# Optimization experiments

Measured on AMD Instinct MI355X. Metric: run time of the kernel, lower is better.

The kernel has to match this reference:

```python
import jax, jax.numpy as jnp
import numpy as np

B = 1024        # number of graphs
MAXLEN = 64     # max nodes per graph (pad_sequence length)
E = 256         # hidden_size
H = 8           # num_heads
HD = E // H     # head dim
NEG = -1e9


def setup_inputs() -> dict:
    key = jax.random.key(0)
    k0, k1, k2 = jax.random.split(key, 3)
    lens = np.tile(np.array([32, 48, 64, 40], dtype=np.int64), B // 4)  # sum = 47104
    batch_indices = jnp.asarray(np.repeat(np.arange(B, dtype=np.int64), lens))
    N = int(lens.sum())
    node_features = jax.random.normal(k0, (N, E), dtype=jnp.float32)
    in_proj_w = jax.random.normal(k1, (3 * E, E), dtype=jnp.float32) * (1.0 / np.sqrt(E))
    in_proj_b = jnp.zeros((3 * E,), dtype=jnp.float32)
    out_proj_w = jax.random.normal(k2, (E, E), dtype=jnp.float32) * (1.0 / np.sqrt(E))
    out_proj_b = jnp.zeros((E,), dtype=jnp.float32)
    return {"node_features": node_features, "batch_indices": batch_indices,
            "in_proj_w": in_proj_w, "in_proj_b": in_proj_b,
            "out_proj_w": out_proj_w, "out_proj_b": out_proj_b}


def _pad_ragged(node_features, batch_indices):
    # counts per graph, start offset of each graph, position of each node in its graph
    N = node_features.shape[0]
    counts = jax.ops.segment_sum(jnp.ones((N,), jnp.int32), batch_indices, num_segments=B)
    starts = jnp.cumsum(counts) - counts
    pos = jnp.arange(N) - starts[batch_indices]
    padded = jnp.zeros((B, MAXLEN, E), node_features.dtype).at[batch_indices, pos].set(node_features)
    key_pad = jnp.arange(MAXLEN)[None, :] >= counts[:, None]  # [B, L] True = padding
    return padded, key_pad


def reference(node_features, batch_indices, in_proj_w, in_proj_b, out_proj_w, out_proj_b):
    padded, key_pad = _pad_ragged(node_features, batch_indices)   # [B,L,E], [B,L]
    qkv = padded @ in_proj_w.T + in_proj_b                        # [B,L,3E]
    q, k, v = jnp.split(qkv, 3, axis=-1)
    q = q.reshape(B, MAXLEN, H, HD)
    k = k.reshape(B, MAXLEN, H, HD)
    v = v.reshape(B, MAXLEN, H, HD)
    scores = jnp.einsum('blhd,bmhd->bhlm', q, k) / jnp.sqrt(jnp.float32(HD))
    scores = jnp.where(key_pad[:, None, None, :], NEG, scores)    # mask padded keys
    attn = jax.nn.softmax(scores, axis=-1)                        # [B,H,L,L]
    ctx = jnp.einsum('bhlm,bmhd->blhd', attn, v).reshape(B, MAXLEN, E)
    out = ctx @ out_proj_w.T + out_proj_b                         # [B,L,E]
    out = jnp.transpose(out, (1, 0, 2))                           # [L,B,E] seq-first like torch
    weights = attn.mean(axis=1)                                   # [B,L,L] head-averaged
    return out, weights
```

## Files before the change

### kernel.cpp

```cpp
#include <hip/hip_runtime.h>

typedef unsigned short u16;
typedef short bf16x8 __attribute__((ext_vector_type(8)));
typedef float f32x4 __attribute__((ext_vector_type(4)));

#define MFMA16(a, b, c) __builtin_amdgcn_mfma_f32_16x16x32_bf16((a), (b), (c), 0, 0, 0)

static __device__ __forceinline__ u16 f2bf(float f) {
    union { float f; unsigned int u; } v; v.f = f;
    unsigned int u = v.u;
    u += 0x7fffu + ((u >> 16) & 1u);
    return (u16)(u >> 16);
}

__global__ void prep_kernel(const int* __restrict__ bidx, int N,
                            const float* __restrict__ w_in, const float* __restrict__ w_out,
                            int* __restrict__ starts, int* __restrict__ counts,
                            u16* __restrict__ w_in_bf, u16* __restrict__ w_out_bf) {
    int tid = blockIdx.x * blockDim.x + threadIdx.x;
    if (tid < 1024) {
        int lo = 0, hi = N;
        while (lo < hi) { int mid = (lo + hi) >> 1; if (bidx[mid] < tid) lo = mid + 1; else hi = mid; }
        int s0 = lo;
        lo = 0; hi = N;
        int v1 = tid + 1;
        while (lo < hi) { int mid = (lo + hi) >> 1; if (bidx[mid] < v1) lo = mid + 1; else hi = mid; }
        starts[tid] = s0;
        counts[tid] = lo - s0;
    }
    {
        float4 v = ((const float4*)w_in)[tid];
        ushort4 o; o.x = f2bf(v.x); o.y = f2bf(v.y); o.z = f2bf(v.z); o.w = f2bf(v.w);
        ((ushort4*)w_in_bf)[tid] = o;
    }
    if (tid < 16384) {
        float4 v = ((const float4*)w_out)[tid];
        ushort4 o; o.x = f2bf(v.x); o.y = f2bf(v.y); o.z = f2bf(v.z); o.w = f2bf(v.w);
        ((ushort4*)w_out_bf)[tid] = o;
    }
}

__global__ __launch_bounds__(256, 2) void gat_kernel(
    const float* __restrict__ X, const float* __restrict__ bias_in,
    const float* __restrict__ bias_out,
    const int* __restrict__ starts, const int* __restrict__ counts,
    const u16* __restrict__ w_in_bf, const u16* __restrict__ w_out_bf,
    float* __restrict__ out, float* __restrict__ wout) {

    __shared__ u16 qg[64][72];
    __shared__ u16 kg[64][72];
    __shared__ u16 vt[64][72];
    __shared__ u16 p_s[4][16][72];
    __shared__ u16 cs[64][264];

    const int b = blockIdx.x;
    const int tid = threadIdx.x;
    const int w = tid >> 6;
    const int lane = tid & 63;
    const int n = lane & 15;
    const int quad = lane >> 4;
    const int s = starts[b];
    const int c = counts[b];
    const int m0 = w * 16;

    bf16x8 afr[4][8];
    #pragma unroll
    for (int st = 0; st < 4; ++st) {
        int row = st * 16 + n;
        bool ok = row < c;
        const float* src = X + (long)(s + row) * 256 + quad * 8;
        #pragma unroll
        for (int ks = 0; ks < 8; ++ks) {
            float4 v0 = make_float4(0.f, 0.f, 0.f, 0.f);
            float4 v1 = make_float4(0.f, 0.f, 0.f, 0.f);
            if (ok) {
                v0 = *(const float4*)(src + ks * 32);
                v1 = *(const float4*)(src + ks * 32 + 4);
            }
            bf16x8 a;
            a[0] = (short)f2bf(v0.x); a[1] = (short)f2bf(v0.y);
            a[2] = (short)f2bf(v0.z); a[3] = (short)f2bf(v0.w);
            a[4] = (short)f2bf(v1.x); a[5] = (short)f2bf(v1.y);
            a[6] = (short)f2bf(v1.z); a[7] = (short)f2bf(v1.w);
            afr[st][ks] = a;
        }
    }

    const float scale = 0.17677669529663687f;
    float wacc[4][4];
    #pragma unroll
    for (int t = 0; t < 4; ++t)
        #pragma unroll
        for (int r = 0; r < 4; ++r) wacc[t][r] = 0.f;

    #pragma unroll 1
    for (int g = 0; g < 4; ++g) {
        #pragma unroll 1
        for (int i = 0; i < 3; ++i) {
            int j = w + i * 4;
            int type = j >> 2;
            int sub = j & 3;
            int wrow = type * 256 + g * 64 + sub * 16 + n;
            bf16x8 bfr[8];
            const u16* wr = w_in_bf + wrow * 256 + quad * 8;
            #pragma unroll
            for (int ks = 0; ks < 8; ++ks) bfr[ks] = *(const bf16x8*)(wr + ks * 32);
            float bias = bias_in[wrow];

            f32x4 acc[4];
            #pragma unroll
            for (int st = 0; st < 4; ++st) acc[st] = (f32x4){0.f, 0.f, 0.f, 0.f};
            #pragma unroll
            for (int ks = 0; ks < 8; ++ks)
                #pragma unroll
                for (int st = 0; st < 4; ++st)
                    acc[st] = MFMA16(afr[st][ks], bfr[ks], acc[st]);

            #pragma unroll
            for (int st = 0; st < 4; ++st) {
                if (type == 2) {
                    ushort4 pk;
                    pk.x = f2bf(acc[st][0] + bias); pk.y = f2bf(acc[st][1] + bias);
                    pk.z = f2bf(acc[st][2] + bias); pk.w = f2bf(acc[st][3] + bias);
                    *(ushort4*)&vt[sub * 16 + n][st * 16 + quad * 4] = pk;
                } else {
                    u16 (*dst)[72] = type ? kg : qg;
                    #pragma unroll
                    for (int r = 0; r < 4; ++r)
                        dst[st * 16 + quad * 4 + r][sub * 16 + n] = f2bf(acc[st][r] + bias);
                }
            }
        }
        __syncthreads();

        #pragma unroll 1
        for (int hh = 0; hh < 2; ++hh) {
            int h = g * 2 + hh;
            bf16x8 aq = *(const bf16x8*)&qg[m0 + n][hh * 32 + quad * 8];
            f32x4 sc[4];
            #pragma unroll
            for (int t = 0; t < 4; ++t) {
                bf16x8 bk = *(const bf16x8*)&kg[t * 16 + n][hh * 32 + quad * 8];
                f32x4 z = (f32x4){0.f, 0.f, 0.f, 0.f};
                sc[t] = MFMA16(aq, bk, z);
            }
            float p[4][4], inv[4];
            #pragma unroll
            for (int r = 0; r < 4; ++r) {
                float mx = -1e30f;
                #pragma unroll
                for (int t = 0; t < 4; ++t) {
                    float sv = ((t * 16 + n) < c) ? sc[t][r] * scale : -1e30f;
                    p[t][r] = sv;
                    mx = fmaxf(mx, sv);
                }
                #pragma unroll
                for (int d = 1; d < 16; d <<= 1) mx = fmaxf(mx, __shfl_xor(mx, d, 64));
                float sm = 0.f;
                #pragma unroll
                for (int t = 0; t < 4; ++t) {
                    float e = ((t * 16 + n) < c) ? __expf(p[t][r] - mx) : 0.f;
                    p[t][r] = e; sm += e;
                }
                #pragma unroll
                for (int d = 1; d < 16; d <<= 1) sm += __shfl_xor(sm, d, 64);
                inv[r] = 1.f / sm;
                #pragma unroll
                for (int t = 0; t < 4; ++t) wacc[t][r] += p[t][r] * (inv[r] * 0.125f);
            }
            #pragma unroll
            for (int t = 0; t < 4; ++t)
                #pragma unroll
                for (int r = 0; r < 4; ++r)
                    p_s[w][quad * 4 + r][t * 16 + n] = f2bf(p[t][r]);
            #pragma unroll
            for (int nt = 0; nt < 2; ++nt) {
                f32x4 acc = (f32x4){0.f, 0.f, 0.f, 0.f};
                #pragma unroll
                for (int k2 = 0; k2 < 2; ++k2) {
                    bf16x8 ap = *(const bf16x8*)&p_s[w][n][k2 * 32 + quad * 8];
                    bf16x8 bv = *(const bf16x8*)&vt[hh * 32 + nt * 16 + n][k2 * 32 + quad * 8];
                    acc = MFMA16(ap, bv, acc);
                }
                #pragma unroll
                for (int r = 0; r < 4; ++r)
                    cs[m0 + quad * 4 + r][h * 32 + nt * 16 + n] = f2bf(acc[r] * inv[r]);
            }
        }
        __syncthreads();
    }

    #pragma unroll
    for (int t = 0; t < 4; ++t)
        #pragma unroll
        for (int r = 0; r < 4; ++r)
            wout[b * 4096 + (m0 + quad * 4 + r) * 64 + t * 16 + n] = wacc[t][r];

    bf16x8 actx[8];
    #pragma unroll
    for (int ks = 0; ks < 8; ++ks)
        actx[ks] = *(const bf16x8*)&cs[m0 + n][ks * 32 + quad * 8];

    #pragma unroll 2
    for (int ct = 0; ct < 16; ++ct) {
        bf16x8 bfr[8];
        const u16* wr = w_out_bf + (ct * 16 + n) * 256 + quad * 8;
        #pragma unroll
        for (int ks = 0; ks < 8; ++ks) bfr[ks] = *(const bf16x8*)(wr + ks * 32);
        f32x4 acc = (f32x4){0.f, 0.f, 0.f, 0.f};
        #pragma unroll
        for (int ks = 0; ks < 8; ++ks) acc = MFMA16(actx[ks], bfr[ks], acc);
        float bias = bias_out[ct * 16 + n];
        #pragma unroll
        for (int r = 0; r < 4; ++r)
            out[(m0 + quad * 4 + r) * 262144 + b * 256 + ct * 16 + n] = acc[r] + bias;
    }
}

extern "C" void kernel_launch(void* const* d_in, const int* in_sizes, int n_in,
                              void* d_out, int out_size, void* d_ws, size_t ws_size,
                              hipStream_t stream) {
    const float* X     = (const float*)d_in[0];
    const int*   bidx  = (const int*)d_in[1];
    const float* w_in  = (const float*)d_in[2];
    const float* b_in  = (const float*)d_in[3];
    const float* w_out = (const float*)d_in[4];
    const float* b_out = (const float*)d_in[5];
    const int N = in_sizes[1];

    float* out  = (float*)d_out;
    float* wout = out + 64 * 1024 * 256;

    int* starts   = (int*)d_ws;
    int* counts   = starts + 1024;
    u16* w_in_bf  = (u16*)(counts + 1024);
    u16* w_out_bf = w_in_bf + 196608;

    hipLaunchKernelGGL(prep_kernel, dim3(192), dim3(256), 0, stream,
                       bidx, N, w_in, w_out, starts, counts, w_in_bf, w_out_bf);
    hipLaunchKernelGGL(gat_kernel, dim3(1024), dim3(256), 0, stream,
                       X, b_in, b_out, starts, counts, w_in_bf, w_out_bf, out, wout);
}
```

Baseline: 281.8 us.

## Split QKV projection by row per wave and keep context in registers

```diff
diff --git a/kernel.cpp b/kernel.cpp
--- a/kernel.cpp
+++ b/kernel.cpp
@@ -40,7 +40,7 @@
     }
 }
 
-__global__ __launch_bounds__(256, 2) void gat_kernel(
+__global__ __launch_bounds__(256, 4) void gat_kernel(
     const float* __restrict__ X, const float* __restrict__ bias_in,
     const float* __restrict__ bias_out,
     const int* __restrict__ starts, const int* __restrict__ counts,
@@ -51,7 +51,6 @@
     __shared__ u16 kg[64][72];
     __shared__ u16 vt[64][72];
     __shared__ u16 p_s[4][16][72];
-    __shared__ u16 cs[64][264];
 
     const int b = blockIdx.x;
     const int tid = threadIdx.x;
@@ -63,10 +62,9 @@
     const int c = counts[b];
     const int m0 = w * 16;
 
-    bf16x8 afr[4][8];
-    #pragma unroll
-    for (int st = 0; st < 4; ++st) {
-        int row = st * 16 + n;
+    bf16x8 afr[8];
+    {
+        int row = m0 + n;
         bool ok = row < c;
         const float* src = X + (long)(s + row) * 256 + quad * 8;
         #pragma unroll
@@ -82,7 +80,7 @@
             a[2] = (short)f2bf(v0.z); a[3] = (short)f2bf(v0.w);
             a[4] = (short)f2bf(v1.x); a[5] = (short)f2bf(v1.y);
             a[6] = (short)f2bf(v1.z); a[7] = (short)f2bf(v1.w);
-            afr[st][ks] = a;
+            afr[ks] = a;
         }
     }
 
@@ -92,50 +90,44 @@
     for (int t = 0; t < 4; ++t)
         #pragma unroll
         for (int r = 0; r < 4; ++r) wacc[t][r] = 0.f;
+    bf16x8 actx[8];
 
     #pragma unroll 1
     for (int g = 0; g < 4; ++g) {
-        #pragma unroll 1
-        for (int i = 0; i < 3; ++i) {
-            int j = w + i * 4;
-            int type = j >> 2;
-            int sub = j & 3;
-            int wrow = type * 256 + g * 64 + sub * 16 + n;
-            bf16x8 bfr[8];
+        #pragma unroll 4
+        for (int j = 0; j < 12; ++j) {
+            const int type = j >> 2;
+            const int sub = j & 3;
+            const int wrow = type * 256 + g * 64 + sub * 16 + n;
             const u16* wr = w_in_bf + wrow * 256 + quad * 8;
-            #pragma unroll
-            for (int ks = 0; ks < 8; ++ks) bfr[ks] = *(const bf16x8*)(wr + ks * 32);
-            float bias = bias_in[wrow];
-
-            f32x4 acc[4];
-            #pragma unroll
-            for (int st = 0; st < 4; ++st) acc[st] = (f32x4){0.f, 0.f, 0.f, 0.f};
-            #pragma unroll
-            for (int ks = 0; ks < 8; ++ks)
-                #pragma unroll
-                for (int st = 0; st < 4; ++st)
-                    acc[st] = MFMA16(afr[st][ks], bfr[ks], acc[st]);
-
-            #pragma unroll
-            for (int st = 0; st < 4; ++st) {
-                if (type == 2) {
-                    ushort4 pk;
-                    pk.x = f2bf(acc[st][0] + bias); pk.y = f2bf(acc[st][1] + bias);
-                    pk.z = f2bf(acc[st][2] + bias); pk.w = f2bf(acc[st][3] + bias);
-                    *(ushort4*)&vt[sub * 16 + n][st * 16 + quad * 4] = pk;
-                } else {
-                    u16 (*dst)[72] = type ? kg : qg;
-                    #pragma unroll
-                    for (int r = 0; r < 4; ++r)
-                        dst[st * 16 + quad * 4 + r][sub * 16 + n] = f2bf(acc[st][r] + bias);
-                }
+            const float bias = bias_in[wrow];
+
+            f32x4 acc = (f32x4){0.f, 0.f, 0.f, 0.f};
+            #pragma unroll
+            for (int kh = 0; kh < 2; ++kh) {
+                bf16x8 bfr[4];
+                #pragma unroll
+                for (int k4 = 0; k4 < 4; ++k4) bfr[k4] = *(const bf16x8*)(wr + (kh * 4 + k4) * 32);
+                #pragma unroll
+                for (int k4 = 0; k4 < 4; ++k4) acc = MFMA16(afr[kh * 4 + k4], bfr[k4], acc);
+            }
+
+            if (type == 2) {
+                ushort4 pk;
+                pk.x = f2bf(acc[0] + bias); pk.y = f2bf(acc[1] + bias);
+                pk.z = f2bf(acc[2] + bias); pk.w = f2bf(acc[3] + bias);
+                *(ushort4*)&vt[sub * 16 + n][m0 + quad * 4] = pk;
+            } else {
+                u16 (*dst)[72] = type ? kg : qg;
+                #pragma unroll
+                for (int r = 0; r < 4; ++r)
+                    dst[m0 + quad * 4 + r][sub * 16 + n] = f2bf(acc[r] + bias);
             }
         }
         __syncthreads();
 
         #pragma unroll 1
         for (int hh = 0; hh < 2; ++hh) {
-            int h = g * 2 + hh;
             bf16x8 aq = *(const bf16x8*)&qg[m0 + n][hh * 32 + quad * 8];
             f32x4 sc[4];
             #pragma unroll
@@ -173,19 +165,22 @@
                 #pragma unroll
                 for (int r = 0; r < 4; ++r)
                     p_s[w][quad * 4 + r][t * 16 + n] = f2bf(p[t][r]);
-            #pragma unroll
-            for (int nt = 0; nt < 2; ++nt) {
-                f32x4 acc = (f32x4){0.f, 0.f, 0.f, 0.f};
-                #pragma unroll
-                for (int k2 = 0; k2 < 2; ++k2) {
-                    bf16x8 ap = *(const bf16x8*)&p_s[w][n][k2 * 32 + quad * 8];
-                    bf16x8 bv = *(const bf16x8*)&vt[hh * 32 + nt * 16 + n][k2 * 32 + quad * 8];
-                    acc = MFMA16(ap, bv, acc);
-                }
-                #pragma unroll
-                for (int r = 0; r < 4; ++r)
-                    cs[m0 + quad * 4 + r][h * 32 + nt * 16 + n] = f2bf(acc[r] * inv[r]);
-            }
+            f32x4 c0 = (f32x4){0.f, 0.f, 0.f, 0.f};
+            f32x4 c1 = (f32x4){0.f, 0.f, 0.f, 0.f};
+            #pragma unroll
+            for (int k2 = 0; k2 < 2; ++k2) {
+                bf16x8 ap  = *(const bf16x8*)&p_s[w][n][k2 * 32 + quad * 8];
+                bf16x8 bv0 = *(const bf16x8*)&vt[hh * 32 + n][k2 * 32 + quad * 8];
+                bf16x8 bv1 = *(const bf16x8*)&vt[hh * 32 + 16 + n][k2 * 32 + quad * 8];
+                c0 = MFMA16(ap, bv0, c0);
+                c1 = MFMA16(ap, bv1, c1);
+            }
+            #pragma unroll
+            for (int r = 0; r < 4; ++r) {
+                p_s[w][quad * 4 + r][n]      = f2bf(c0[r] * inv[r]);
+                p_s[w][quad * 4 + r][16 + n] = f2bf(c1[r] * inv[r]);
+            }
+            actx[g * 2 + hh] = *(const bf16x8*)&p_s[w][n][quad * 8];
         }
         __syncthreads();
     }
@@ -195,11 +190,6 @@
         #pragma unroll
         for (int r = 0; r < 4; ++r)
             wout[b * 4096 + (m0 + quad * 4 + r) * 64 + t * 16 + n] = wacc[t][r];
-
-    bf16x8 actx[8];
-    #pragma unroll
-    for (int ks = 0; ks < 8; ++ks)
-        actx[ks] = *(const bf16x8*)&cs[m0 + n][ks * 32 + quad * 8];
 
     #pragma unroll 2
     for (int ct = 0; ct < 16; ++ct) {
```

New measurement: 367.7 us. +30.5%, slower.

## Double block to 512 threads and split work across eight waves

Applied to the files above, without the earlier changes.

```diff
diff --git a/kernel.cpp b/kernel.cpp
--- a/kernel.cpp
+++ b/kernel.cpp
@@ -40,7 +40,7 @@
     }
 }
 
-__global__ __launch_bounds__(256, 2) void gat_kernel(
+__global__ __launch_bounds__(512, 2) void gat_kernel(
     const float* __restrict__ X, const float* __restrict__ bias_in,
     const float* __restrict__ bias_out,
     const int* __restrict__ starts, const int* __restrict__ counts,
@@ -50,7 +50,7 @@
     __shared__ u16 qg[64][72];
     __shared__ u16 kg[64][72];
     __shared__ u16 vt[64][72];
-    __shared__ u16 p_s[4][16][72];
+    __shared__ u16 p_s[8][16][72];
     __shared__ u16 cs[64][264];
 
     const int b = blockIdx.x;
@@ -61,12 +61,17 @@
     const int quad = lane >> 4;
     const int s = starts[b];
     const int c = counts[b];
-    const int m0 = w * 16;
-
-    bf16x8 afr[4][8];
+
+    const int wh = w >> 2;
+    const int wj = w & 3;
+    const int hh = w & 1;
+    const int rt = w >> 1;
+    const int m0 = rt * 16;
+
+    bf16x8 afr[2][8];
     #pragma unroll
-    for (int st = 0; st < 4; ++st) {
-        int row = st * 16 + n;
+    for (int st2 = 0; st2 < 2; ++st2) {
+        int row = wh * 32 + st2 * 16 + n;
         bool ok = row < c;
         const float* src = X + (long)(s + row) * 256 + quad * 8;
         #pragma unroll
@@ -82,7 +87,7 @@
             a[2] = (short)f2bf(v0.z); a[3] = (short)f2bf(v0.w);
             a[4] = (short)f2bf(v1.x); a[5] = (short)f2bf(v1.y);
             a[6] = (short)f2bf(v1.z); a[7] = (short)f2bf(v1.w);
-            afr[st][ks] = a;
+            afr[st2][ks] = a;
         }
     }
 
@@ -95,47 +100,47 @@
 
     #pragma unroll 1
     for (int g = 0; g < 4; ++g) {
-        #pragma unroll 1
+        #pragma unroll
         for (int i = 0; i < 3; ++i) {
-            int j = w + i * 4;
-            int type = j >> 2;
-            int sub = j & 3;
-            int wrow = type * 256 + g * 64 + sub * 16 + n;
-            bf16x8 bfr[8];
+            const int wrow = i * 256 + g * 64 + wj * 16 + n;
             const u16* wr = w_in_bf + wrow * 256 + quad * 8;
-            #pragma unroll
-            for (int ks = 0; ks < 8; ++ks) bfr[ks] = *(const bf16x8*)(wr + ks * 32);
-            float bias = bias_in[wrow];
-
-            f32x4 acc[4];
-            #pragma unroll
-            for (int st = 0; st < 4; ++st) acc[st] = (f32x4){0.f, 0.f, 0.f, 0.f};
-            #pragma unroll
-            for (int ks = 0; ks < 8; ++ks)
-                #pragma unroll
-                for (int st = 0; st < 4; ++st)
-                    acc[st] = MFMA16(afr[st][ks], bfr[ks], acc[st]);
-
-            #pragma unroll
-            for (int st = 0; st < 4; ++st) {
-                if (type == 2) {
+            const float bias = bias_in[wrow];
+
+            f32x4 acc[2];
+            acc[0] = (f32x4){0.f, 0.f, 0.f, 0.f};
+            acc[1] = (f32x4){0.f, 0.f, 0.f, 0.f};
+            #pragma unroll
+            for (int kh = 0; kh < 2; ++kh) {
+                bf16x8 bfr[4];
+                #pragma unroll
+                for (int k4 = 0; k4 < 4; ++k4) bfr[k4] = *(const bf16x8*)(wr + (kh * 4 + k4) * 32);
+                #pragma unroll
+                for (int k4 = 0; k4 < 4; ++k4) {
+                    acc[0] = MFMA16(afr[0][kh * 4 + k4], bfr[k4], acc[0]);
+                    acc[1] = MFMA16(afr[1][kh * 4 + k4], bfr[k4], acc[1]);
+                }
+            }
+
+            #pragma unroll
+            for (int st2 = 0; st2 < 2; ++st2) {
+                const int st = 2 * wh + st2;
+                if (i == 2) {
                     ushort4 pk;
-                    pk.x = f2bf(acc[st][0] + bias); pk.y = f2bf(acc[st][1] + bias);
-                    pk.z = f2bf(acc[st][2] + bias); pk.w = f2bf(acc[st][3] + bias);
-                    *(ushort4*)&vt[sub * 16 + n][st * 16 + quad * 4] = pk;
+                    pk.x = f2bf(acc[st2][0] + bias); pk.y = f2bf(acc[st2][1] + bias);
+                    pk.z = f2bf(acc[st2][2] + bias); pk.w = f2bf(acc[st2][3] + bias);
+                    *(ushort4*)&vt[wj * 16 + n][st * 16 + quad * 4] = pk;
                 } else {
-                    u16 (*dst)[72] = type ? kg : qg;
+                    u16 (*dst)[72] = i ? kg : qg;
                     #pragma unroll
                     for (int r = 0; r < 4; ++r)
-                        dst[st * 16 + quad * 4 + r][sub * 16 + n] = f2bf(acc[st][r] + bias);
+                        dst[st * 16 + quad * 4 + r][wj * 16 + n] = f2bf(acc[st2][r] + bias);
                 }
             }
         }
         __syncthreads();
 
-        #pragma unroll 1
-        for (int hh = 0; hh < 2; ++hh) {
-            int h = g * 2 + hh;
+        {
+            const int h = g * 2 + hh;
             bf16x8 aq = *(const bf16x8*)&qg[m0 + n][hh * 32 + quad * 8];
             f32x4 sc[4];
             #pragma unroll
@@ -190,30 +195,63 @@
         __syncthreads();
     }
 
-    #pragma unroll
-    for (int t = 0; t < 4; ++t)
-        #pragma unroll
-        for (int r = 0; r < 4; ++r)
-            wout[b * 4096 + (m0 + quad * 4 + r) * 64 + t * 16 + n] = wacc[t][r];
-
-    bf16x8 actx[8];
-    #pragma unroll
-    for (int ks = 0; ks < 8; ++ks)
-        actx[ks] = *(const bf16x8*)&cs[m0 + n][ks * 32 + quad * 8];
-
-    #pragma unroll 2
-    for (int ct = 0; ct < 16; ++ct) {
-        bf16x8 bfr[8];
-        const u16* wr = w_out_bf + (ct * 16 + n) * 256 + quad * 8;
-        #pragma unroll
-        for (int ks = 0; ks < 8; ++ks) bfr[ks] = *(const bf16x8*)(wr + ks * 32);
-        f32x4 acc = (f32x4){0.f, 0.f, 0.f, 0.f};
-        #pragma unroll
-        for (int ks = 0; ks < 8; ++ks) acc = MFMA16(actx[ks], bfr[ks], acc);
-        float bias = bias_out[ct * 16 + n];
-        #pragma unroll
-        for (int r = 0; r < 4; ++r)
-            out[(m0 + quad * 4 + r) * 262144 + b * 256 + ct * 16 + n] = acc[r] + bias;
+    {
+        float* pw = (float*)&p_s[w & ~1][0][0];
+        if (hh == 0) {
+            #pragma unroll
+            for (int t = 0; t < 4; ++t)
+                #pragma unroll
+                for (int r = 0; r < 4; ++r)
+                    pw[(quad * 4 + r) * 64 + t * 16 + n] = wacc[t][r];
+        }
+        __syncthreads();
+        if (hh == 1) {
+            #pragma unroll
+            for (int t = 0; t < 4; ++t)
+                #pragma unroll
+                for (int r = 0; r < 4; ++r)
+                    wout[b * 4096 + (m0 + quad * 4 + r) * 64 + t * 16 + n] =
+                        wacc[t][r] + pw[(quad * 4 + r) * 64 + t * 16 + n];
+        }
+    }
+
+    {
+        const int sp = w & 1;
+        const int cq = w >> 1;
+        bf16x8 actx[2][8];
+        #pragma unroll
+        for (int st2 = 0; st2 < 2; ++st2)
+            #pragma unroll
+            for (int ks = 0; ks < 8; ++ks)
+                actx[st2][ks] = *(const bf16x8*)&cs[(2 * sp + st2) * 16 + n][ks * 32 + quad * 8];
+
+        #pragma unroll 2
+        for (int ci = 0; ci < 4; ++ci) {
+            const int ct = 4 * cq + ci;
+            const u16* wr = w_out_bf + (ct * 16 + n) * 256 + quad * 8;
+            f32x4 acc[2];
+            acc[0] = (f32x4){0.f, 0.f, 0.f, 0.f};
+            acc[1] = (f32x4){0.f, 0.f, 0.f, 0.f};
+            #pragma unroll
+            for (int kh = 0; kh < 2; ++kh) {
+                bf16x8 bfr[4];
+                #pragma unroll
+                for (int k4 = 0; k4 < 4; ++k4) bfr[k4] = *(const bf16x8*)(wr + (kh * 4 + k4) * 32);
+                #pragma unroll
+                for (int k4 = 0; k4 < 4; ++k4) {
+                    acc[0] = MFMA16(actx[0][kh * 4 + k4], bfr[k4], acc[0]);
+                    acc[1] = MFMA16(actx[1][kh * 4 + k4], bfr[k4], acc[1]);
+                }
+            }
+            float bias = bias_out[ct * 16 + n];
+            #pragma unroll
+            for (int st2 = 0; st2 < 2; ++st2) {
+                const int orow = (2 * sp + st2) * 16 + quad * 4;
+                #pragma unroll
+                for (int r = 0; r < 4; ++r)
+                    out[(orow + r) * 262144 + b * 256 + ct * 16 + n] = acc[st2][r] + bias;
+            }
+        }
     }
 }
 
@@ -238,6 +276,6 @@
 
     hipLaunchKernelGGL(prep_kernel, dim3(192), dim3(256), 0, stream,
                        bidx, N, w_in, w_out, starts, counts, w_in_bf, w_out_bf);
-    hipLaunchKernelGGL(gat_kernel, dim3(1024), dim3(256), 0, stream,
+    hipLaunchKernelGGL(gat_kernel, dim3(1024), dim3(512), 0, stream,
                        X, b_in, b_out, starts, counts, w_in_bf, w_out_bf, out, wout);
 }
```

Measured after the change: 293.7 us. +4.2%, slower.
